# Kernel optimization log

Measured on AMD Instinct MI355X. Metric: run time of the kernel, lower is better.

Reference implementation:

```python
import jax, jax.numpy as jnp
import numpy as np


def _conv1x1(x, w, b):
    # x: [B,C,H,W], w: [O,C], b: [O] -> [B,O,H,W]
    return jnp.einsum('oc,bchw->bohw', w, x) + b[None, :, None, None]


def setup_inputs() -> dict:
    key = jax.random.key(0)
    ks = jax.random.split(key, 9)
    B, C, O, H, W = 8, 192, 96, 64, 64
    s_in = 1.0 / np.sqrt(C)
    s_out = 1.0 / np.sqrt(O)
    return {
        'x': jax.random.normal(ks[0], (B, C, H, W), dtype=jnp.float32),
        'g_w': jax.random.normal(ks[1], (O, C), dtype=jnp.float32) * s_in,
        'g_b': jax.random.normal(ks[2], (O,), dtype=jnp.float32) * s_in,
        'theta_w': jax.random.normal(ks[3], (O, C), dtype=jnp.float32) * s_in,
        'theta_b': jax.random.normal(ks[4], (O,), dtype=jnp.float32) * s_in,
        'phi_w': jax.random.normal(ks[5], (O, C), dtype=jnp.float32) * s_in,
        'phi_b': jax.random.normal(ks[6], (O,), dtype=jnp.float32) * s_in,
        'W_w': jax.random.normal(ks[7], (C, O), dtype=jnp.float32) * s_out,
        'W_b': jax.random.normal(ks[8], (C,), dtype=jnp.float32) * s_out,
    }


def reference(x, g_w, g_b, theta_w, theta_b, phi_w, phi_b, W_w, W_b):
    B, C, H, W = x.shape
    O = g_w.shape[0]
    N = H * W
    # 1x1 conv projections, flattened to [B, O, N]
    g_x = _conv1x1(x, g_w, g_b).reshape(B, O, N)          # [B,O,N]
    theta_x = _conv1x1(x, theta_w, theta_b).reshape(B, O, N)
    phi_x = _conv1x1(x, phi_w, phi_b).reshape(B, O, N)
    # scores f1[b,n,m] = theta[:, :, n] . phi[:, :, m]
    f1 = jnp.einsum('bon,bom->bnm', theta_x, phi_x)       # [B,N,N]
    f_div_C = jax.nn.softmax(f1, axis=-1)
    # y[b,n,o] = sum_m f[b,n,m] * g[b,o,m]
    y = jnp.einsum('bnm,bom->bon', f_div_C, g_x)          # [B,O,N]
    y = y.reshape(B, O, H, W)
    W_y = _conv1x1(y, W_w, W_b)                           # [B,C,H,W]
    return W_y + x
```

## Files before the change

kernel.cpp:

```cpp
#include <hip/hip_runtime.h>

typedef unsigned short u16;
typedef unsigned int u32;
typedef float f32x4 __attribute__((ext_vector_type(4)));
typedef float f32x16 __attribute__((ext_vector_type(16)));
typedef _Float16 h16x8 __attribute__((ext_vector_type(8)));
typedef u32 u32x4 __attribute__((ext_vector_type(4)));
typedef u32 u32x2 __attribute__((ext_vector_type(2)));
typedef u16 u16x4 __attribute__((ext_vector_type(4)));

#define NB 8
#define CC 192
#define OO 96
#define NN 4096
#define NSPLIT 4
#define XPAD 200
#define LOG2E 1.4426950408889634f

static __device__ __forceinline__ u16 f2h(float f) {
  _Float16 h = (_Float16)f;
  return __builtin_bit_cast(u16, h);
}
static __device__ __forceinline__ void gl_lds16(const u16* g, u16* l) {
  __builtin_amdgcn_global_load_lds(
      (const __attribute__((address_space(1))) void*)g,
      (__attribute__((address_space(3))) void*)l, 16, 0, 0);
}
static __device__ __forceinline__ float exp2_raw(float x) {
  float r;
  asm("v_exp_f32 %0, %1" : "=v"(r) : "v"(x));
  return r;
}
static __device__ __forceinline__ void plane_swap(u32& a, u32& b) {
  u32x2 r = __builtin_amdgcn_permlane32_swap(a, b, false, false);
  a = r[0]; b = r[1];
}
static __device__ __forceinline__ float half_combine_max(float x) {
  u32 a = __builtin_bit_cast(u32, x), b = a;
  plane_swap(a, b);
  return fmaxf(__builtin_bit_cast(float, a), __builtin_bit_cast(float, b));
}
static __device__ __forceinline__ float half_combine_sum(float x) {
  u32 a = __builtin_bit_cast(u32, x), b = a;
  plane_swap(a, b);
  return __builtin_bit_cast(float, a) + __builtin_bit_cast(float, b);
}
static __device__ __forceinline__ float max3f(float a, float b, float c) {
  return fmaxf(fmaxf(a, b), c);
}

__global__ __launch_bounds__(256) void proj_kernel(
    const float* __restrict__ x,
    const float* __restrict__ g_w, const float* __restrict__ g_b,
    const float* __restrict__ th_w, const float* __restrict__ th_b,
    const float* __restrict__ ph_w, const float* __restrict__ ph_b,
    u16* __restrict__ QB, u16* __restrict__ KA, u16* __restrict__ VA)
{
  __shared__ __align__(16) u16 Xs[64][XPAD];
  __shared__ __align__(16) u16 Ws[96][XPAD];
  const int b = blockIdx.y, n0 = blockIdx.x * 64, tid = threadIdx.x;
  const int lane = tid & 63, wv = tid >> 6, l15 = lane & 15, lg = lane >> 4;

  #pragma unroll
  for (int it = 0; it < 12; ++it) {
    int idx = tid + it * 256;
    int c = idx >> 4, q = idx & 15;
    float4 v = *(const float4*)(x + ((size_t)(b * CC + c)) * NN + n0 + q * 4);
    Xs[q * 4 + 0][c] = f2h(v.x); Xs[q * 4 + 1][c] = f2h(v.y);
    Xs[q * 4 + 2][c] = f2h(v.z); Xs[q * 4 + 3][c] = f2h(v.w);
  }

  for (int p = 0; p < 3; ++p) {
    const float* w    = (p == 0) ? th_w : (p == 1) ? ph_w : g_w;
    const float* bias = (p == 0) ? th_b : (p == 1) ? ph_b : g_b;
    const float scale = (p == 0) ? LOG2E : 1.0f;
    __syncthreads();
    #pragma unroll
    for (int it = 0; it < 18; ++it) {
      int idx = tid + it * 256;
      int r = idx / 48, q = idx % 48;
      float4 v = *(const float4*)(w + r * CC + q * 4);
      u16x4 hh; hh[0] = f2h(v.x * scale); hh[1] = f2h(v.y * scale);
      hh[2] = f2h(v.z * scale); hh[3] = f2h(v.w * scale);
      *(u16x4*)&Ws[r][q * 4] = hh;
    }
    __syncthreads();

    f32x4 acc[6];
    #pragma unroll
    for (int of = 0; of < 6; ++of) acc[of] = (f32x4){0.f, 0.f, 0.f, 0.f};
    #pragma unroll
    for (int ks = 0; ks < 6; ++ks) {
      h16x8 xa = *(const h16x8*)&Xs[wv * 16 + l15][ks * 32 + lg * 8];
      #pragma unroll
      for (int of = 0; of < 6; ++of) {
        h16x8 wf = *(const h16x8*)&Ws[of * 16 + l15][ks * 32 + lg * 8];
        if (p < 2) acc[of] = __builtin_amdgcn_mfma_f32_16x16x32_f16(xa, wf, acc[of], 0, 0, 0);
        else       acc[of] = __builtin_amdgcn_mfma_f32_16x16x32_f16(wf, xa, acc[of], 0, 0, 0);
      }
    }

    if (p < 2) {
      u16* dst = (p == 0) ? QB : KA;
      #pragma unroll
      for (int of = 0; of < 6; ++of) {
        int o = of * 16 + l15;
        float bo = bias[o] * scale;
        int kch = of * 2 + (l15 >> 3);
        #pragma unroll
        for (int r = 0; r < 4; ++r) {
          int n = n0 + wv * 16 + lg * 4 + r;
          int idx = (b * 128 + (n >> 5)) * 3072 + (kch * 32 + (n & 31)) * 8 + (o & 7);
          dst[idx] = f2h(acc[of][r] + bo);
        }
      }
    } else {
      #pragma unroll
      for (int of = 0; of < 6; ++of) {
        #pragma unroll
        for (int r = 0; r < 4; ++r) {
          int o = of * 16 + lg * 4 + r;
          int m = n0 + wv * 16 + l15;
          int idx = (b * 256 + (m >> 4)) * 1536 +
                    (((o >> 5) * 2 + ((m >> 3) & 1)) * 32 + (o & 31)) * 8 + (m & 7);
          VA[idx] = f2h(acc[of][r] + bias[o]);
        }
      }
    }
  }
}

__global__ __launch_bounds__(128, 2) void attn_kernel(
    const u16* __restrict__ QB, const u16* __restrict__ KA,
    const u16* __restrict__ VA, u16* __restrict__ yP, float* __restrict__ ml)
{
  __shared__ __align__(16) u16 Ks[6144];
  __shared__ __align__(16) u16 Vs[6144];
  const int b   = blockIdx.x;
  const int qt  = blockIdx.y;
  const int sp  = blockIdx.z;
  const int tid = threadIdx.x;
  const int lane = tid & 63;
  const int wv  = tid >> 6;
  const int l31 = lane & 31;
  const int h   = lane >> 5;

  const int t_start = 16 * sp;
  const int t_end   = 16 * (sp + 1);

  const int ncA = qt * 4 + wv * 2;
  const int ncB = ncA + 1;
  const u16* qbA = QB + (size_t)(b * 128 + ncA) * 3072;
  const u16* qbB = QB + (size_t)(b * 128 + ncB) * 3072;
  h16x8 qfA[6], qfB[6];
  #pragma unroll
  for (int ks = 0; ks < 6; ++ks) {
    qfA[ks] = *(const h16x8*)(qbA + ((ks * 2 + h) * 32 + l31) * 8);
    qfB[ks] = *(const h16x8*)(qbB + ((ks * 2 + h) * 32 + l31) * 8);
  }

  const u16* gk = KA + (size_t)b * (128 * 3072) + (size_t)t_start * 6144;
  const u16* gv = VA + (size_t)b * (256 * 1536) + (size_t)t_start * 6144;

  f32x16 accA[3], accB[3];
  #pragma unroll
  for (int ob = 0; ob < 3; ++ob)
    #pragma unroll
    for (int i = 0; i < 16; ++i) { accA[ob][i] = 0.f; accB[ob][i] = 0.f; }
  float mA = -3.0e38f, lA = 0.f;
  float mB = -3.0e38f, lB = 0.f;

  for (int t = t_start; t < t_end; ++t) {
    #pragma unroll
    for (int i = 0; i < 6; ++i) gl_lds16(gk + tid * 8 + i * 1024, &Ks[tid * 8 + i * 1024]);
    #pragma unroll
    for (int i = 0; i < 6; ++i) gl_lds16(gv + tid * 8 + i * 1024, &Vs[tid * 8 + i * 1024]);
    gk += 6144; gv += 6144;
    asm volatile("s_waitcnt vmcnt(0)" ::: "memory");
    __builtin_amdgcn_s_barrier();
    __builtin_amdgcn_sched_barrier(0);

    #pragma unroll
    for (int c = 0; c < 2; ++c) {
      const u16* kc = &Ks[c * 3072];
      const u16* vc = &Vs[c * 3072];
      f32x16 SA, SB;
      #pragma unroll
      for (int i = 0; i < 16; ++i) { SA[i] = 0.f; SB[i] = 0.f; }
      #pragma unroll
      for (int ks = 0; ks < 6; ++ks) {
        h16x8 kf = *(const h16x8*)(kc + ((ks * 2 + h) * 32 + l31) * 8);
        SA = __builtin_amdgcn_mfma_f32_32x32x16_f16(kf, qfA[ks], SA, 0, 0, 0);
        SB = __builtin_amdgcn_mfma_f32_32x32x16_f16(kf, qfB[ks], SB, 0, 0, 0);
      }

      u32 pkA[8];
      {
        float t0 = max3f(SA[0], SA[1], SA[2]),   t1 = max3f(SA[3], SA[4], SA[5]);
        float t2 = max3f(SA[6], SA[7], SA[8]),   t3 = max3f(SA[9], SA[10], SA[11]);
        float t4 = max3f(SA[12], SA[13], SA[14]);
        float pmax = half_combine_max(fmaxf(max3f(t0, t1, t2), max3f(t3, t4, SA[15])));
        if (__ballot(pmax > mA + 11.5416f)) {
          float mn = fmaxf(mA, pmax);
          float sc = exp2_raw(mA - mn);
          mA = mn; lA *= sc;
          #pragma unroll
          for (int ob = 0; ob < 3; ++ob)
            #pragma unroll
            for (int i = 0; i < 16; ++i) accA[ob][i] *= sc;
        }
        #pragma unroll
        for (int i = 0; i < 16; ++i) SA[i] = exp2_raw(SA[i] - mA);
        #pragma unroll
        for (int i = 0; i < 8; ++i)
          pkA[i] = __builtin_bit_cast(u32, __builtin_amdgcn_cvt_pkrtz(SA[2 * i], SA[2 * i + 1]));
        #pragma unroll
        for (int st = 8; st >= 1; st >>= 1)
          #pragma unroll
          for (int i = 0; i < 8; ++i) if (i < st) SA[i] += SA[i + st];
        lA += half_combine_sum(SA[0]);
        plane_swap(pkA[0], pkA[2]); plane_swap(pkA[1], pkA[3]);
        plane_swap(pkA[4], pkA[6]); plane_swap(pkA[5], pkA[7]);
      }
      u32 pkB[8];
      {
        float t0 = max3f(SB[0], SB[1], SB[2]),   t1 = max3f(SB[3], SB[4], SB[5]);
        float t2 = max3f(SB[6], SB[7], SB[8]),   t3 = max3f(SB[9], SB[10], SB[11]);
        float t4 = max3f(SB[12], SB[13], SB[14]);
        float pmax = half_combine_max(fmaxf(max3f(t0, t1, t2), max3f(t3, t4, SB[15])));
        if (__ballot(pmax > mB + 11.5416f)) {
          float mn = fmaxf(mB, pmax);
          float sc = exp2_raw(mB - mn);
          mB = mn; lB *= sc;
          #pragma unroll
          for (int ob = 0; ob < 3; ++ob)
            #pragma unroll
            for (int i = 0; i < 16; ++i) accB[ob][i] *= sc;
        }
        #pragma unroll
        for (int i = 0; i < 16; ++i) SB[i] = exp2_raw(SB[i] - mB);
        #pragma unroll
        for (int i = 0; i < 8; ++i)
          pkB[i] = __builtin_bit_cast(u32, __builtin_amdgcn_cvt_pkrtz(SB[2 * i], SB[2 * i + 1]));
        #pragma unroll
        for (int st = 8; st >= 1; st >>= 1)
          #pragma unroll
          for (int i = 0; i < 8; ++i) if (i < st) SB[i] += SB[i + st];
        lB += half_combine_sum(SB[0]);
        plane_swap(pkB[0], pkB[2]); plane_swap(pkB[1], pkB[3]);
        plane_swap(pkB[4], pkB[6]); plane_swap(pkB[5], pkB[7]);
      }
      u32x4 a0 = {pkA[0], pkA[1], pkA[2], pkA[3]}, a1 = {pkA[4], pkA[5], pkA[6], pkA[7]};
      u32x4 b0 = {pkB[0], pkB[1], pkB[2], pkB[3]}, b1 = {pkB[4], pkB[5], pkB[6], pkB[7]};
      h16x8 pfA[2] = {__builtin_bit_cast(h16x8, a0), __builtin_bit_cast(h16x8, a1)};
      h16x8 pfB[2] = {__builtin_bit_cast(h16x8, b0), __builtin_bit_cast(h16x8, b1)};

      #pragma unroll
      for (int s2 = 0; s2 < 2; ++s2) {
        #pragma unroll
        for (int ob = 0; ob < 3; ++ob) {
          h16x8 vf = *(const h16x8*)(vc + (((s2 * 3 + ob) * 2 + h) * 32 + l31) * 8);
          accA[ob] = __builtin_amdgcn_mfma_f32_32x32x16_f16(vf, pfA[s2], accA[ob], 0, 0, 0);
          accB[ob] = __builtin_amdgcn_mfma_f32_32x32x16_f16(vf, pfB[s2], accB[ob], 0, 0, 0);
        }
      }
    }
    __builtin_amdgcn_s_barrier();
  }

  #pragma unroll
  for (int qq = 0; qq < 2; ++qq) {
    const f32x16* acc = qq ? accB : accA;
    float mR = qq ? mB : mA, lR = qq ? lB : lA;
    float inv = 1.0f / lR;
    int nglob = (qq ? ncB : ncA) * 32 + l31;
    u16* yp = yP + (((size_t)sp * NB + b) * NN + nglob) * OO;
    #pragma unroll
    for (int ob = 0; ob < 3; ++ob) {
      #pragma unroll
      for (int rq = 0; rq < 4; ++rq) {
        int o0 = ob * 32 + rq * 8 + h * 4;
        u32 w0 = __builtin_bit_cast(u32,
            __builtin_amdgcn_cvt_pkrtz(acc[ob][rq * 4 + 0] * inv, acc[ob][rq * 4 + 1] * inv));
        u32 w1 = __builtin_bit_cast(u32,
            __builtin_amdgcn_cvt_pkrtz(acc[ob][rq * 4 + 2] * inv, acc[ob][rq * 4 + 3] * inv));
        uint2 pr; pr.x = w0; pr.y = w1;
        *(uint2*)&yp[o0] = pr;
      }
    }
    if (h == 0) {
      float2 v2; v2.x = mR; v2.y = lR;
      *(float2*)&ml[(((size_t)sp * NB + b) * NN + nglob) * 2] = v2;
    }
  }
}

#define YPAD 104
__global__ __launch_bounds__(256) void outproj_kernel(
    const float* __restrict__ x, const float* __restrict__ Ww,
    const float* __restrict__ Wb, const u16* __restrict__ yP,
    const float* __restrict__ ml, float* __restrict__ out)
{
  __shared__ __align__(16) u16 Wws[CC][YPAD];
  __shared__ __align__(16) u16 Ys[64][YPAD];
  const int b = blockIdx.y, n0 = blockIdx.x * 64, tid = threadIdx.x;
  const int lane = tid & 63, wv = tid >> 6, l15 = lane & 15, lg = lane >> 4;
  const size_t SB = (size_t)NB * NN;

  #pragma unroll
  for (int it = 0; it < 18; ++it) {
    int idx = tid + it * 256;
    int r = idx / 24, q = idx % 24;
    float4 v = *(const float4*)(Ww + r * OO + q * 4);
    u16x4 hh; hh[0] = f2h(v.x); hh[1] = f2h(v.y); hh[2] = f2h(v.z); hh[3] = f2h(v.w);
    *(u16x4*)&Wws[r][q * 4] = hh;
  }
  #pragma unroll
  for (int it = 0; it < 3; ++it) {
    int idx = tid + it * 256;
    int n = idx / 12, q = idx % 12;
    size_t bn = (size_t)b * NN + n0 + n;
    float mm[NSPLIT], ll[NSPLIT];
    float M = -3.0e38f;
    #pragma unroll
    for (int s = 0; s < NSPLIT; ++s) {
      mm[s] = ml[((size_t)s * SB + bn) * 2];
      ll[s] = ml[((size_t)s * SB + bn) * 2 + 1];
      M = fmaxf(M, mm[s]);
    }
    float wsum = 0.f, w[NSPLIT];
    #pragma unroll
    for (int s = 0; s < NSPLIT; ++s) { w[s] = ll[s] * exp2f(mm[s] - M); wsum += w[s]; }
    float rinv = 1.0f / wsum;
    #pragma unroll
    for (int s = 0; s < NSPLIT; ++s) w[s] *= rinv;
    float accv[8];
    #pragma unroll
    for (int e = 0; e < 8; ++e) accv[e] = 0.f;
    #pragma unroll
    for (int s = 0; s < NSPLIT; ++s) {
      h16x8 ys = *(const h16x8*)(yP + ((size_t)s * SB + bn) * OO + q * 8);
      #pragma unroll
      for (int e = 0; e < 8; ++e) accv[e] += w[s] * (float)ys[e];
    }
    u32x4 packed;
    #pragma unroll
    for (int e = 0; e < 4; ++e)
      packed[e] = __builtin_bit_cast(u32,
          __builtin_amdgcn_cvt_pkrtz(accv[2 * e], accv[2 * e + 1]));
    *(u32x4*)&Ys[n][q * 8] = packed;
  }
  __syncthreads();

  f32x4 acc[12];
  #pragma unroll
  for (int cf = 0; cf < 12; ++cf) acc[cf] = (f32x4){0.f, 0.f, 0.f, 0.f};
  #pragma unroll
  for (int ks = 0; ks < 3; ++ks) {
    h16x8 yb = *(const h16x8*)&Ys[wv * 16 + l15][ks * 32 + lg * 8];
    #pragma unroll
    for (int cf = 0; cf < 12; ++cf) {
      h16x8 wa = *(const h16x8*)&Wws[cf * 16 + l15][ks * 32 + lg * 8];
      acc[cf] = __builtin_amdgcn_mfma_f32_16x16x32_f16(wa, yb, acc[cf], 0, 0, 0);
    }
  }
  #pragma unroll
  for (int cf = 0; cf < 12; ++cf) {
    #pragma unroll
    for (int r = 0; r < 4; ++r) {
      int c = cf * 16 + lg * 4 + r;
      size_t off = ((size_t)(b * CC + c)) * NN + n0 + wv * 16 + l15;
      out[off] = acc[cf][r] + x[off] + Wb[c];
    }
  }
}

extern "C" void kernel_launch(void* const* d_in, const int* in_sizes, int n_in,
                              void* d_out, int out_size, void* d_ws, size_t ws_size,
                              hipStream_t stream) {
  const float* x    = (const float*)d_in[0];
  const float* g_w  = (const float*)d_in[1];
  const float* g_b  = (const float*)d_in[2];
  const float* th_w = (const float*)d_in[3];
  const float* th_b = (const float*)d_in[4];
  const float* ph_w = (const float*)d_in[5];
  const float* ph_b = (const float*)d_in[6];
  const float* W_w  = (const float*)d_in[7];
  const float* W_b  = (const float*)d_in[8];
  float* out = (float*)d_out;

  char* ws = (char*)d_ws;
  const size_t projB = (size_t)NB * NN * OO * sizeof(u16);
  u16* QB   = (u16*)ws;
  u16* KA   = (u16*)(ws + projB);
  u16* VA   = (u16*)(ws + 2 * projB);
  u16* yP   = (u16*)(ws + 3 * projB);
  float* ml = (float*)(ws + (3 + NSPLIT) * projB);

  dim3 gproj(64, NB);
  hipLaunchKernelGGL(proj_kernel, gproj, dim3(256), 0, stream,
                     x, g_w, g_b, th_w, th_b, ph_w, ph_b, QB, KA, VA);
  dim3 gattn(NB, 32, NSPLIT);
  hipLaunchKernelGGL(attn_kernel, gattn, dim3(128), 0, stream, QB, KA, VA, yP, ml);
  dim3 gout(64, NB);
  hipLaunchKernelGGL(outproj_kernel, gout, dim3(256), 0, stream, x, W_w, W_b, yP, ml, out);
}
```

Baseline: 97.84 us.

## Use one query tile per wave with 256-thread attention blocks

The attention kernel now gives each wave a single 32-row query tile instead of two, and uses 4 waves per block (256 threads) rather than 2. This cuts per-thread register use (one accumulator set and one softmax state), which allows higher occupancy under launch_bounds(256,4). The K/V tile loaded into LDS is shared across more waves, so each thread issues fewer loads. The cost is that each K/V fragment read from LDS now feeds only one MFMA instead of two, so MFMA-level interleaving drops and LDS read traffic per unit of compute rises.

```diff
diff --git a/kernel.cpp b/kernel.cpp
--- a/kernel.cpp
+++ b/kernel.cpp
@@ -130,7 +130,66 @@
   }
 }
 
-__global__ __launch_bounds__(128, 2) void attn_kernel(
+static __device__ __forceinline__ void qk_one(
+    const u16* kc, const h16x8* qf, int h, int l31, f32x16& S)
+{
+  #pragma unroll
+  for (int i = 0; i < 16; ++i) S[i] = 0.f;
+  #pragma unroll
+  for (int ks = 0; ks < 6; ++ks) {
+    h16x8 kf = *(const h16x8*)(kc + ((ks * 2 + h) * 32 + l31) * 8);
+    S = __builtin_amdgcn_mfma_f32_32x32x16_f16(kf, qf[ks], S, 0, 0, 0);
+  }
+}
+
+static __device__ __forceinline__ void sm_one(
+    f32x16 S, float& m, float& l, f32x16* acc, h16x8* pf)
+{
+  float a0 = max3f(S[0], S[1], S[2]),  a1 = max3f(S[3], S[4], S[5]);
+  float a2 = max3f(S[6], S[7], S[8]),  a3 = max3f(S[9], S[10], S[11]);
+  float a4 = max3f(S[12], S[13], S[14]);
+  float pmax = half_combine_max(fmaxf(max3f(a0, a1, a2), max3f(a3, a4, S[15])));
+  if (__ballot(pmax > m + 11.5416f)) {
+    float mn = fmaxf(m, pmax);
+    float sc = exp2_raw(m - mn);
+    m = mn; l *= sc;
+    #pragma unroll
+    for (int ob = 0; ob < 3; ++ob)
+      #pragma unroll
+      for (int i = 0; i < 16; ++i) acc[ob][i] *= sc;
+  }
+  #pragma unroll
+  for (int i = 0; i < 16; ++i) S[i] = exp2_raw(S[i] - m);
+  u32 pk[8];
+  #pragma unroll
+  for (int i = 0; i < 8; ++i)
+    pk[i] = __builtin_bit_cast(u32, __builtin_amdgcn_cvt_pkrtz(S[2 * i], S[2 * i + 1]));
+  #pragma unroll
+  for (int st = 8; st >= 1; st >>= 1)
+    #pragma unroll
+    for (int i = 0; i < 8; ++i)
+      if (i < st) S[i] += S[i + st];
+  l += half_combine_sum(S[0]);
+  plane_swap(pk[0], pk[2]); plane_swap(pk[1], pk[3]);
+  plane_swap(pk[4], pk[6]); plane_swap(pk[5], pk[7]);
+  u32x4 v0 = {pk[0], pk[1], pk[2], pk[3]}, v1 = {pk[4], pk[5], pk[6], pk[7]};
+  pf[0] = __builtin_bit_cast(h16x8, v0); pf[1] = __builtin_bit_cast(h16x8, v1);
+}
+
+static __device__ __forceinline__ void pv_one(
+    const u16* vc, const h16x8* pf, int h, int l31, f32x16* acc)
+{
+  #pragma unroll
+  for (int s2 = 0; s2 < 2; ++s2) {
+    #pragma unroll
+    for (int ob = 0; ob < 3; ++ob) {
+      h16x8 vf = *(const h16x8*)(vc + (((s2 * 3 + ob) * 2 + h) * 32 + l31) * 8);
+      acc[ob] = __builtin_amdgcn_mfma_f32_32x32x16_f16(vf, pf[s2], acc[ob], 0, 0, 0);
+    }
+  }
+}
+
+__global__ __launch_bounds__(256, 4) void attn_kernel(
     const u16* __restrict__ QB, const u16* __restrict__ KA,
     const u16* __restrict__ VA, u16* __restrict__ yP, float* __restrict__ ml)
 {
@@ -148,33 +207,28 @@
   const int t_start = 16 * sp;
   const int t_end   = 16 * (sp + 1);
 
-  const int ncA = qt * 4 + wv * 2;
-  const int ncB = ncA + 1;
-  const u16* qbA = QB + (size_t)(b * 128 + ncA) * 3072;
-  const u16* qbB = QB + (size_t)(b * 128 + ncB) * 3072;
-  h16x8 qfA[6], qfB[6];
-  #pragma unroll
-  for (int ks = 0; ks < 6; ++ks) {
-    qfA[ks] = *(const h16x8*)(qbA + ((ks * 2 + h) * 32 + l31) * 8);
-    qfB[ks] = *(const h16x8*)(qbB + ((ks * 2 + h) * 32 + l31) * 8);
-  }
+  const int nc = qt * 4 + wv;
+  const u16* qb = QB + (size_t)(b * 128 + nc) * 3072;
+  h16x8 qf[6];
+  #pragma unroll
+  for (int ks = 0; ks < 6; ++ks)
+    qf[ks] = *(const h16x8*)(qb + ((ks * 2 + h) * 32 + l31) * 8);
 
   const u16* gk = KA + (size_t)b * (128 * 3072) + (size_t)t_start * 6144;
   const u16* gv = VA + (size_t)b * (256 * 1536) + (size_t)t_start * 6144;
 
-  f32x16 accA[3], accB[3];
+  f32x16 acc[3];
   #pragma unroll
   for (int ob = 0; ob < 3; ++ob)
     #pragma unroll
-    for (int i = 0; i < 16; ++i) { accA[ob][i] = 0.f; accB[ob][i] = 0.f; }
-  float mA = -3.0e38f, lA = 0.f;
-  float mB = -3.0e38f, lB = 0.f;
+    for (int i = 0; i < 16; ++i) acc[ob][i] = 0.f;
+  float m = -3.0e38f, l = 0.f;
 
   for (int t = t_start; t < t_end; ++t) {
     #pragma unroll
-    for (int i = 0; i < 6; ++i) gl_lds16(gk + tid * 8 + i * 1024, &Ks[tid * 8 + i * 1024]);
-    #pragma unroll
-    for (int i = 0; i < 6; ++i) gl_lds16(gv + tid * 8 + i * 1024, &Vs[tid * 8 + i * 1024]);
+    for (int i = 0; i < 3; ++i) gl_lds16(gk + tid * 8 + i * 2048, &Ks[tid * 8 + i * 2048]);
+    #pragma unroll
+    for (int i = 0; i < 3; ++i) gl_lds16(gv + tid * 8 + i * 2048, &Vs[tid * 8 + i * 2048]);
     gk += 6144; gv += 6144;
     asm volatile("s_waitcnt vmcnt(0)" ::: "memory");
     __builtin_amdgcn_s_barrier();
@@ -182,98 +236,18 @@
 
     #pragma unroll
     for (int c = 0; c < 2; ++c) {
-      const u16* kc = &Ks[c * 3072];
-      const u16* vc = &Vs[c * 3072];
-      f32x16 SA, SB;
-      #pragma unroll
-      for (int i = 0; i < 16; ++i) { SA[i] = 0.f; SB[i] = 0.f; }
-      #pragma unroll
-      for (int ks = 0; ks < 6; ++ks) {
-        h16x8 kf = *(const h16x8*)(kc + ((ks * 2 + h) * 32 + l31) * 8);
-        SA = __builtin_amdgcn_mfma_f32_32x32x16_f16(kf, qfA[ks], SA, 0, 0, 0);
-        SB = __builtin_amdgcn_mfma_f32_32x32x16_f16(kf, qfB[ks], SB, 0, 0, 0);
-      }
-
-      u32 pkA[8];
-      {
-        float t0 = max3f(SA[0], SA[1], SA[2]),   t1 = max3f(SA[3], SA[4], SA[5]);
-        float t2 = max3f(SA[6], SA[7], SA[8]),   t3 = max3f(SA[9], SA[10], SA[11]);
-        float t4 = max3f(SA[12], SA[13], SA[14]);
-        float pmax = half_combine_max(fmaxf(max3f(t0, t1, t2), max3f(t3, t4, SA[15])));
-        if (__ballot(pmax > mA + 11.5416f)) {
-          float mn = fmaxf(mA, pmax);
-          float sc = exp2_raw(mA - mn);
-          mA = mn; lA *= sc;
-          #pragma unroll
-          for (int ob = 0; ob < 3; ++ob)
-            #pragma unroll
-            for (int i = 0; i < 16; ++i) accA[ob][i] *= sc;
-        }
-        #pragma unroll
-        for (int i = 0; i < 16; ++i) SA[i] = exp2_raw(SA[i] - mA);
-        #pragma unroll
-        for (int i = 0; i < 8; ++i)
-          pkA[i] = __builtin_bit_cast(u32, __builtin_amdgcn_cvt_pkrtz(SA[2 * i], SA[2 * i + 1]));
-        #pragma unroll
-        for (int st = 8; st >= 1; st >>= 1)
-          #pragma unroll
-          for (int i = 0; i < 8; ++i) if (i < st) SA[i] += SA[i + st];
-        lA += half_combine_sum(SA[0]);
-        plane_swap(pkA[0], pkA[2]); plane_swap(pkA[1], pkA[3]);
-        plane_swap(pkA[4], pkA[6]); plane_swap(pkA[5], pkA[7]);
-      }
-      u32 pkB[8];
-      {
-        float t0 = max3f(SB[0], SB[1], SB[2]),   t1 = max3f(SB[3], SB[4], SB[5]);
-        float t2 = max3f(SB[6], SB[7], SB[8]),   t3 = max3f(SB[9], SB[10], SB[11]);
-        float t4 = max3f(SB[12], SB[13], SB[14]);
-        float pmax = half_combine_max(fmaxf(max3f(t0, t1, t2), max3f(t3, t4, SB[15])));
-        if (__ballot(pmax > mB + 11.5416f)) {
-          float mn = fmaxf(mB, pmax);
-          float sc = exp2_raw(mB - mn);
-          mB = mn; lB *= sc;
-          #pragma unroll
-          for (int ob = 0; ob < 3; ++ob)
-            #pragma unroll
-            for (int i = 0; i < 16; ++i) accB[ob][i] *= sc;
-        }
-        #pragma unroll
-        for (int i = 0; i < 16; ++i) SB[i] = exp2_raw(SB[i] - mB);
-        #pragma unroll
-        for (int i = 0; i < 8; ++i)
-          pkB[i] = __builtin_bit_cast(u32, __builtin_amdgcn_cvt_pkrtz(SB[2 * i], SB[2 * i + 1]));
-        #pragma unroll
-        for (int st = 8; st >= 1; st >>= 1)
-          #pragma unroll
-          for (int i = 0; i < 8; ++i) if (i < st) SB[i] += SB[i + st];
-        lB += half_combine_sum(SB[0]);
-        plane_swap(pkB[0], pkB[2]); plane_swap(pkB[1], pkB[3]);
-        plane_swap(pkB[4], pkB[6]); plane_swap(pkB[5], pkB[7]);
-      }
-      u32x4 a0 = {pkA[0], pkA[1], pkA[2], pkA[3]}, a1 = {pkA[4], pkA[5], pkA[6], pkA[7]};
-      u32x4 b0 = {pkB[0], pkB[1], pkB[2], pkB[3]}, b1 = {pkB[4], pkB[5], pkB[6], pkB[7]};
-      h16x8 pfA[2] = {__builtin_bit_cast(h16x8, a0), __builtin_bit_cast(h16x8, a1)};
-      h16x8 pfB[2] = {__builtin_bit_cast(h16x8, b0), __builtin_bit_cast(h16x8, b1)};
-
-      #pragma unroll
-      for (int s2 = 0; s2 < 2; ++s2) {
-        #pragma unroll
-        for (int ob = 0; ob < 3; ++ob) {
-          h16x8 vf = *(const h16x8*)(vc + (((s2 * 3 + ob) * 2 + h) * 32 + l31) * 8);
-          accA[ob] = __builtin_amdgcn_mfma_f32_32x32x16_f16(vf, pfA[s2], accA[ob], 0, 0, 0);
-          accB[ob] = __builtin_amdgcn_mfma_f32_32x32x16_f16(vf, pfB[s2], accB[ob], 0, 0, 0);
-        }
-      }
+      f32x16 S;
+      h16x8 pf[2];
+      qk_one(&Ks[c * 3072], qf, h, l31, S);
+      sm_one(S, m, l, acc, pf);
+      pv_one(&Vs[c * 3072], pf, h, l31, acc);
     }
     __builtin_amdgcn_s_barrier();
   }
 
-  #pragma unroll
-  for (int qq = 0; qq < 2; ++qq) {
-    const f32x16* acc = qq ? accB : accA;
-    float mR = qq ? mB : mA, lR = qq ? lB : lA;
-    float inv = 1.0f / lR;
-    int nglob = (qq ? ncB : ncA) * 32 + l31;
+  {
+    float inv = 1.0f / l;
+    int nglob = nc * 32 + l31;
     u16* yp = yP + (((size_t)sp * NB + b) * NN + nglob) * OO;
     #pragma unroll
     for (int ob = 0; ob < 3; ++ob) {
@@ -289,7 +263,7 @@
       }
     }
     if (h == 0) {
-      float2 v2; v2.x = mR; v2.y = lR;
+      float2 v2; v2.x = m; v2.y = l;
       *(float2*)&ml[(((size_t)sp * NB + b) * NN + nglob) * 2] = v2;
     }
   }
@@ -401,7 +375,7 @@
   hipLaunchKernelGGL(proj_kernel, gproj, dim3(256), 0, stream,
                      x, g_w, g_b, th_w, th_b, ph_w, ph_b, QB, KA, VA);
   dim3 gattn(NB, 32, NSPLIT);
-  hipLaunchKernelGGL(attn_kernel, gattn, dim3(128), 0, stream, QB, KA, VA, yP, ml);
+  hipLaunchKernelGGL(attn_kernel, gattn, dim3(256), 0, stream, QB, KA, VA, yP, ml);
   dim3 gout(64, NB);
   hipLaunchKernelGGL(outproj_kernel, gout, dim3(256), 0, stream, x, W_w, W_b, yP, ml, out);
 }
```

Result: no change. 98.80 us (+1.0%).
